# Performance work log

Hardware: AMD Instinct MI355X
Metric: run time of the kernel (lower is better)

The kernel has to match this reference:

```python
import jax, jax.numpy as jnp
import numpy as np

HIDDEN = 2048
NUM_HEADS = 16
NUM_KV_HEADS = 8
HEAD_DIM = 128
EPS = 1e-6
ROPE_THETA = 10000.0
Q_SIZE = NUM_HEADS * HEAD_DIM
KV_SIZE = NUM_KV_HEADS * HEAD_DIM


def setup_inputs() -> dict:
    key = jax.random.key(0)
    k1, k2, k3 = jax.random.split(key, 3)
    B, S = 2, 2048
    positions = jnp.broadcast_to(jnp.arange(S, dtype=jnp.int32), (B, S))
    hidden_states = jax.random.normal(k1, (B, S, HIDDEN), dtype=jnp.float32)
    w_qkv = jax.random.normal(k2, (Q_SIZE + 2 * KV_SIZE, HIDDEN), dtype=jnp.float32) * (HIDDEN ** -0.5)
    w_o = jax.random.normal(k3, (HIDDEN, Q_SIZE), dtype=jnp.float32) * (Q_SIZE ** -0.5)
    q_norm_w = jnp.ones((HEAD_DIM,), dtype=jnp.float32)
    k_norm_w = jnp.ones((HEAD_DIM,), dtype=jnp.float32)
    return {"positions": positions, "hidden_states": hidden_states,
            "w_qkv": w_qkv, "w_o": w_o, "q_norm_w": q_norm_w, "k_norm_w": k_norm_w}


def _rms_norm(x, w):
    # x: [..., HEAD_DIM]
    var = jnp.mean(x * x, axis=-1, keepdims=True)
    return x * jax.lax.rsqrt(var + EPS) * w


def _rope(x, cos, sin):
    # x: [B, S, H, D]; cos/sin: [B, S, 1, D/2] (neox style: rotate half)
    x1, x2 = jnp.split(x, 2, axis=-1)
    return jnp.concatenate([x1 * cos - x2 * sin, x2 * cos + x1 * sin], axis=-1)


def reference(positions, hidden_states, w_qkv, w_o, q_norm_w, k_norm_w):
    B, S, _ = hidden_states.shape
    qkv = jnp.einsum("bsh,oh->bso", hidden_states, w_qkv)
    q, k, v = jnp.split(qkv, [Q_SIZE, Q_SIZE + KV_SIZE], axis=-1)
    q = q.reshape(B, S, NUM_HEADS, HEAD_DIM)
    k = k.reshape(B, S, NUM_KV_HEADS, HEAD_DIM)
    v = v.reshape(B, S, NUM_KV_HEADS, HEAD_DIM)

    # per-head RMSNorm on q and k (Qwen3 qk-norm)
    q = _rms_norm(q, q_norm_w)
    k = _rms_norm(k, k_norm_w)

    # RoPE (neox style)
    inv_freq = 1.0 / (ROPE_THETA ** (jnp.arange(0, HEAD_DIM, 2, dtype=jnp.float32) / HEAD_DIM))
    angles = positions.astype(jnp.float32)[..., None] * inv_freq  # [B, S, D/2]
    cos = jnp.cos(angles)[:, :, None, :]
    sin = jnp.sin(angles)[:, :, None, :]
    q = _rope(q, cos, sin)
    k = _rope(k, cos, sin)

    # GQA: expand kv heads to match q heads
    rep = NUM_HEADS // NUM_KV_HEADS
    k = jnp.repeat(k, rep, axis=2)  # [B, S, H, D]
    v = jnp.repeat(v, rep, axis=2)

    scale = HEAD_DIM ** -0.5
    scores = jnp.einsum("bqhd,bkhd->bhqk", q, k) * scale
    causal = jnp.tril(jnp.ones((S, S), dtype=bool))
    scores = jnp.where(causal, scores, jnp.finfo(scores.dtype).min)
    probs = jax.nn.softmax(scores, axis=-1)
    attn = jnp.einsum("bhqk,bkhd->bqhd", probs, v).reshape(B, S, Q_SIZE)
    return jnp.einsum("bso,ho->bsh", attn, w_o)
```

## Files before the change

kernel.cpp:

```cpp
#include <hip/hip_runtime.h>
#include <hip/hip_bf16.h>
#include <cstdint>
#include <cstddef>

#define HIDDEN 2048
#define NHEADS 16
#define NKV    8
#define HD     128
#define QS     (NHEADS*HD)
#define KVS    (NKV*HD)
#define OC     (QS + 2*KVS)
#define BB     2
#define SS     2048
#define ROWS   (BB*SS)

typedef __bf16 bf16;
typedef __bf16 bf16x8 __attribute__((ext_vector_type(8)));
typedef __bf16 bf16x4 __attribute__((ext_vector_type(4)));
typedef float  f32x4  __attribute__((ext_vector_type(4)));
typedef float  f32x2  __attribute__((ext_vector_type(2)));
typedef int    i32x4  __attribute__((ext_vector_type(4)));

__global__ __launch_bounds__(256) void k_cvt(const float* __restrict__ src,
                                             bf16* __restrict__ dst, int n8) {
  int i = blockIdx.x * blockDim.x + threadIdx.x;
  int stride = gridDim.x * blockDim.x;
  for (; i < n8; i += stride) {
    const f32x4* s = (const f32x4*)(src + (size_t)i * 8);
    f32x4 a = s[0], b = s[1];
    bf16x8 o;
    o[0]=(bf16)a[0]; o[1]=(bf16)a[1]; o[2]=(bf16)a[2]; o[3]=(bf16)a[3];
    o[4]=(bf16)b[0]; o[5]=(bf16)b[1]; o[6]=(bf16)b[2]; o[7]=(bf16)b[3];
    *(bf16x8*)(dst + (size_t)i * 8) = o;
  }
}

__global__ __launch_bounds__(256) void k_table(float* __restrict__ tbl) {
  int t = blockIdx.x * blockDim.x + threadIdx.x;
  int pos = t >> 6, i = t & 63;
  float freq = powf(10000.0f, -(float)i / 64.0f);
  float ang = (float)pos * freq;
  float sv, cv;
  sincosf(ang, &sv, &cv);
  f32x2 v; v[0] = cv; v[1] = sv;
  ((f32x2*)tbl)[t] = v;
}

__device__ __forceinline__ void gll16(const void* g, void* l) {
  __builtin_amdgcn_global_load_lds((const __attribute__((address_space(1))) void*)g,
                                   (__attribute__((address_space(3))) void*)l, 16, 0, 0);
}

template <typename OT>
__global__ __launch_bounds__(256) void k_gemm(const bf16* __restrict__ A,
                                              const bf16* __restrict__ Bw,
                                              OT* __restrict__ C,
                                              int M, int N, int K) {
  const int tid = threadIdx.x;
  const int lane = tid & 63;
  const int w = tid >> 6;
  const int m0 = blockIdx.y * 128, n0 = blockIdx.x * 128;
  __shared__ bf16 As[128 * 64];
  __shared__ bf16 Bs[128 * 64];
  f32x4 acc[4][4] = {};
  const int wm = (w >> 1) * 64, wn = (w & 1) * 64;
  const int lr = lane & 15, lg = lane >> 4;
  const int KT = K >> 6;
  for (int kt = 0; kt < KT; ++kt) {
    __syncthreads();
    #pragma unroll
    for (int i = 0; i < 4; ++i) {
      int c = tid + i * 256;
      int row = c >> 3, kc = c & 7;
      int ch = kc ^ (row & 7);
      gll16(A + (size_t)(m0 + row) * K + kt * 64 + ch * 8, As + (size_t)(c & ~63) * 8);
      gll16(Bw + (size_t)(n0 + row) * K + kt * 64 + ch * 8, Bs + (size_t)(c & ~63) * 8);
    }
    asm volatile("s_waitcnt vmcnt(0)" ::: "memory");
    __syncthreads();
    #pragma unroll
    for (int kh = 0; kh < 2; ++kh) {
      bf16x8 af[4], bfv[4];
      #pragma unroll
      for (int i = 0; i < 4; ++i) {
        int row = wm + i * 16 + lr;
        af[i] = *(const bf16x8*)((char*)As + ((row * 128 + kh * 64 + lg * 16) ^ ((lr & 7) << 4)));
      }
      #pragma unroll
      for (int j = 0; j < 4; ++j) {
        int row = wn + j * 16 + lr;
        bfv[j] = *(const bf16x8*)((char*)Bs + ((row * 128 + kh * 64 + lg * 16) ^ ((lr & 7) << 4)));
      }
      #pragma unroll
      for (int i = 0; i < 4; ++i)
        #pragma unroll
        for (int j = 0; j < 4; ++j)
          acc[i][j] = __builtin_amdgcn_mfma_f32_16x16x32_bf16(af[i], bfv[j], acc[i][j], 0, 0, 0);
    }
  }
  for (int i = 0; i < 4; ++i)
    for (int j = 0; j < 4; ++j) {
      int col = n0 + wn + j * 16 + lr;
      for (int r = 0; r < 4; ++r) {
        int row = m0 + wm + i * 16 + lg * 4 + r;
        C[(size_t)row * N + col] = (OT)acc[i][j][r];
      }
    }
}

__global__ __launch_bounds__(256) void k_ropenorm(const bf16* __restrict__ qkv,
                                                  bf16* __restrict__ qb, bf16* __restrict__ kb,
                                                  const float* __restrict__ tbl,
                                                  const int* __restrict__ pos,
                                                  const float* __restrict__ qw,
                                                  const float* __restrict__ kw) {
  int gw = blockIdx.x * 4 + (threadIdx.x >> 6);
  int lane = threadIdx.x & 63;
  int h = gw % 24;
  int rem = gw / 24;
  int s = rem & (SS - 1);
  int b = rem >> 11;
  size_t row = (size_t)b * SS + s;
  int col0 = (h < 16) ? h * HD : QS + (h - 16) * HD;
  unsigned u = *(const unsigned*)(qkv + row * OC + col0 + lane * 2);
  float x0 = __uint_as_float((u & 0xffffu) << 16);
  float x1 = __uint_as_float(u & 0xffff0000u);
  float ssq = x0 * x0 + x1 * x1;
  for (int m = 1; m < 64; m <<= 1) ssq += __shfl_xor(ssq, m, 64);
  float r = rsqrtf(ssq * (1.0f / 128.0f) + 1e-6f);
  const float* wv = (h < 16) ? qw : kw;
  float y0 = x0 * r * wv[lane * 2], y1 = x1 * r * wv[lane * 2 + 1];
  float p0 = __shfl_xor(y0, 32, 64), p1 = __shfl_xor(y1, 32, 64);
  int p = pos[row];
  f32x4 cs = *(const f32x4*)(tbl + (size_t)p * 128 + (lane & 31) * 4);
  float o0, o1;
  if (lane < 32) { o0 = y0 * cs[0] - p0 * cs[1]; o1 = y1 * cs[2] - p1 * cs[3]; }
  else           { o0 = y0 * cs[0] + p0 * cs[1]; o1 = y1 * cs[2] + p1 * cs[3]; }
  bf16* dst; size_t drow;
  if (h < 16) { dst = qb; drow = ((size_t)b * NHEADS + h) * SS + s; }
  else        { dst = kb; drow = ((size_t)b * NKV + (h - 16)) * SS + s; }
  bf16 v0 = (bf16)o0, v1 = (bf16)o1;
  unsigned short q0, q1;
  __builtin_memcpy(&q0, &v0, 2); __builtin_memcpy(&q1, &v1, 2);
  *(unsigned*)(dst + drow * HD + lane * 2) = (unsigned)q0 | ((unsigned)q1 << 16);
}

__global__ __launch_bounds__(256) void k_vt(const bf16* __restrict__ qkv,
                                            bf16* __restrict__ vT) {
  __shared__ bf16 T[64 * 136];
  int tid = threadIdx.x;
  int st = blockIdx.x, kv = blockIdx.y, b = blockIdx.z;
  int s0 = st * 64;
  for (int i = 0; i < 4; ++i) {
    int c = tid + i * 256;
    int sl = c >> 4, dc = c & 15;
    i32x4 v = *(const i32x4*)(qkv + (size_t)(b * SS + s0 + sl) * OC + QS + KVS + kv * HD + dc * 8);
    *(i32x4*)(T + sl * 136 + dc * 8) = v;
  }
  __syncthreads();
  for (int i = 0; i < 4; ++i) {
    int c = tid + i * 256;
    int d = c >> 3, sg = c & 7;
    bf16x8 o;
    for (int j = 0; j < 8; ++j) o[j] = T[(sg * 8 + j) * 136 + d];
    *(bf16x8*)(vT + ((size_t)(b * NKV + kv) * HD + d) * SS + s0 + sg * 8) = o;
  }
}

__global__ __launch_bounds__(256) void k_attn9(const bf16* __restrict__ qb,
                                               const bf16* __restrict__ kb,
                                               const bf16* __restrict__ vT,
                                               bf16* __restrict__ out) {
  __shared__ bf16 Kl[64 * 128];
  __shared__ bf16 Vl[128 * 64];
  __shared__ bf16 Pl[4][16 * 64];
  const int tid = threadIdx.x, lane = tid & 63, w = tid >> 6;
  const int qt = gridDim.x - 1 - blockIdx.x;
  const int h = blockIdx.y, b = blockIdx.z;
  const int kvh = h >> 1;
  const int lr = lane & 15, lg = lane >> 4;
  const int qbase = qt * 64 + w * 16;
  const float NEG = -3.0e38f;
  bf16x8 qf[4];
  {
    const bf16* qrow = qb + ((size_t)(b * NHEADS + h) * SS + qbase + lr) * HD;
    #pragma unroll
    for (int ks = 0; ks < 4; ++ks) qf[ks] = *(const bf16x8*)(qrow + ks * 32 + lg * 8);
  }
  f32x4 acc[8] = {};
  float m_r = NEG, l_r = 0.0f;
  const bf16* Kg = kb + (size_t)(b * NKV + kvh) * SS * HD;
  const bf16* Vg = vT + (size_t)(b * NKV + kvh) * HD * SS;
  for (int t = 0; t <= qt; ++t) {
    const int kv0 = t * 64;
    __syncthreads();
    #pragma unroll
    for (int i = 0; i < 4; ++i) {
      int c = tid + i * 256;
      int r_ = c >> 4;
      int ch = (c & 15) ^ (r_ & 7);
      gll16(Kg + (size_t)(kv0 + r_) * HD + ch * 8, Kl + (size_t)(c & ~63) * 8);
    }
    #pragma unroll
    for (int i = 0; i < 4; ++i) {
      int c = tid + i * 256;
      int d = c >> 3;
      int ch = (c & 7) ^ (d & 7);
      gll16(Vg + (size_t)d * SS + kv0 + ch * 8, Vl + (size_t)(c & ~63) * 8);
    }
    asm volatile("s_waitcnt vmcnt(0)" ::: "memory");
    __syncthreads();
    f32x4 sf[4];
    __builtin_amdgcn_s_setprio(1);
    #pragma unroll
    for (int mt = 0; mt < 4; ++mt) {
      f32x4 a_ = {0.f, 0.f, 0.f, 0.f};
      const int rrow = mt * 16 + lr;
      #pragma unroll
      for (int ks = 0; ks < 4; ++ks) {
        bf16x8 kf = *(const bf16x8*)((char*)Kl + ((rrow * 256 + ks * 64 + lg * 16) ^ ((rrow & 7) << 4)));
        a_ = __builtin_amdgcn_mfma_f32_16x16x32_bf16(kf, qf[ks], a_, 0, 0, 0);
      }
      sf[mt] = a_;
    }
    __builtin_amdgcn_s_setprio(0);
    const float scl = 0.08838834764831845f;
    const int qg = qbase + lr;
    float pm = NEG;
    #pragma unroll
    for (int mt = 0; mt < 4; ++mt)
      #pragma unroll
      for (int r = 0; r < 4; ++r) {
        int kvg = kv0 + mt * 16 + lg * 4 + r;
        float v = sf[mt][r] * scl;
        if (kvg > qg) v = NEG;
        sf[mt][r] = v;
        pm = fmaxf(pm, v);
      }
    pm = fmaxf(pm, __shfl_xor(pm, 16, 64));
    pm = fmaxf(pm, __shfl_xor(pm, 32, 64));
    if (!__all(pm <= m_r + 8.0f)) {
      const float mn = fmaxf(m_r, pm);
      const float scale = __expf(m_r - mn);
      float sr[4];
      #pragma unroll
      for (int r = 0; r < 4; ++r) sr[r] = __shfl(scale, lg * 4 + r, 64);
      #pragma unroll
      for (int nt = 0; nt < 8; ++nt)
        #pragma unroll
        for (int r = 0; r < 4; ++r) acc[nt][r] *= sr[r];
      l_r *= scale;
      m_r = mn;
    }
    float ts = 0.f;
    #pragma unroll
    for (int mt = 0; mt < 4; ++mt)
      #pragma unroll
      for (int r = 0; r < 4; ++r) {
        float pv = __expf(sf[mt][r] - m_r);
        sf[mt][r] = pv;
        ts += pv;
      }
    ts += __shfl_xor(ts, 16, 64);
    ts += __shfl_xor(ts, 32, 64);
    l_r += ts;
    #pragma unroll
    for (int mt = 0; mt < 4; ++mt) {
      bf16x4 pk;
      #pragma unroll
      for (int r = 0; r < 4; ++r) pk[r] = (bf16)sf[mt][r];
      *(bf16x4*)((char*)&Pl[w][0] + ((lr * 128 + mt * 32 + lg * 8) ^ ((lr & 7) << 4))) = pk;
    }
    __builtin_amdgcn_s_setprio(1);
    #pragma unroll
    for (int kk = 0; kk < 2; ++kk) {
      bf16x8 pa = *(const bf16x8*)((char*)&Pl[w][0] + ((lr * 128 + kk * 64 + lg * 16) ^ ((lr & 7) << 4)));
      #pragma unroll
      for (int nt = 0; nt < 8; ++nt) {
        const int d = nt * 16 + lr;
        bf16x8 vbf = *(const bf16x8*)((char*)Vl + ((d * 128 + kk * 64 + lg * 16) ^ ((d & 7) << 4)));
        acc[nt] = __builtin_amdgcn_mfma_f32_16x16x32_bf16(pa, vbf, acc[nt], 0, 0, 0);
      }
    }
    __builtin_amdgcn_s_setprio(0);
  }
  const float inv = 1.0f / l_r;
  float ir[4];
  #pragma unroll
  for (int r = 0; r < 4; ++r) ir[r] = __shfl(inv, lg * 4 + r, 64);
  #pragma unroll
  for (int nt = 0; nt < 8; ++nt)
    #pragma unroll
    for (int r = 0; r < 4; ++r) {
      size_t row = (size_t)b * SS + qbase + lg * 4 + r;
      out[row * QS + h * HD + nt * 16 + lr] = (bf16)(acc[nt][r] * ir[r]);
    }
}

extern "C" void kernel_launch(void* const* d_in, const int* in_sizes, int n_in,
                              void* d_out, int out_size, void* d_ws, size_t ws_size,
                              hipStream_t stream) {
  const int*   pos  = (const int*)d_in[0];
  const float* hid  = (const float*)d_in[1];
  const float* wqkv = (const float*)d_in[2];
  const float* wo   = (const float*)d_in[3];
  const float* qw   = (const float*)d_in[4];
  const float* kw   = (const float*)d_in[5];
  char* ws = (char*)d_ws;
  bf16* hid_bf  = (bf16*)(ws + 0);
  bf16* attn_o  = hid_bf;
  bf16* wqkv_bf = (bf16*)(ws + 16777216);
  bf16* q_buf   = wqkv_bf;
  bf16* k_buf   = (bf16*)(ws + 33554432);
  bf16* wo_bf   = k_buf;
  bf16* qkv     = (bf16*)(ws + 41943040);
  bf16* vT      = (bf16*)(ws + 75497472);
  float* tbl    = (float*)(ws + 83886080);

  k_cvt<<<dim3(2048), dim3(256), 0, stream>>>(hid,  hid_bf,  ROWS * HIDDEN / 8);
  k_cvt<<<dim3(2048), dim3(256), 0, stream>>>(wqkv, wqkv_bf, OC * HIDDEN / 8);
  k_table<<<dim3(512), dim3(256), 0, stream>>>(tbl);
  k_gemm<bf16><<<dim3(OC / 128, ROWS / 128), dim3(256), 0, stream>>>(
      hid_bf, wqkv_bf, qkv, ROWS, OC, HIDDEN);
  k_ropenorm<<<dim3(ROWS * 24 / 4), dim3(256), 0, stream>>>(
      qkv, q_buf, k_buf, tbl, pos, qw, kw);
  k_vt<<<dim3(SS / 64, NKV, BB), dim3(256), 0, stream>>>(qkv, vT);
  k_attn9<<<dim3(SS / 64, NHEADS, BB), dim3(256), 0, stream>>>(
      q_buf, k_buf, vT, attn_o);
  k_cvt<<<dim3(2048), dim3(256), 0, stream>>>(wo, wo_bf, HIDDEN * QS / 8);
  k_gemm<float><<<dim3(HIDDEN / 128, ROWS / 128), dim3(256), 0, stream>>>(
      attn_o, wo_bf, (float*)d_out, ROWS, HIDDEN, QS);
}
```

Baseline: 302.8 us.

## Use 32x32 MFMA in GEMM, exp2 softmax, and merge conversion launches

```diff
diff --git a/kernel.cpp b/kernel.cpp
--- a/kernel.cpp
+++ b/kernel.cpp
@@ -19,6 +19,7 @@
 typedef __bf16 bf16x4 __attribute__((ext_vector_type(4)));
 typedef float  f32x4  __attribute__((ext_vector_type(4)));
 typedef float  f32x2  __attribute__((ext_vector_type(2)));
+typedef float  f32x16 __attribute__((ext_vector_type(16)));
 typedef int    i32x4  __attribute__((ext_vector_type(4)));
 
 __global__ __launch_bounds__(256) void k_cvt(const float* __restrict__ src,
@@ -35,6 +36,24 @@
   }
 }
 
+__global__ __launch_bounds__(256) void k_cvt2(const float* __restrict__ s0, bf16* __restrict__ d0, int n0,
+                                              const float* __restrict__ s1, bf16* __restrict__ d1, int n1) {
+  int i = blockIdx.x * blockDim.x + threadIdx.x;
+  int stride = gridDim.x * blockDim.x;
+  int total = n0 + n1;
+  for (; i < total; i += stride) {
+    const float* src; bf16* dst; int k;
+    if (i < n0) { src = s0; dst = d0; k = i; }
+    else        { src = s1; dst = d1; k = i - n0; }
+    const f32x4* s = (const f32x4*)(src + (size_t)k * 8);
+    f32x4 a = s[0], b = s[1];
+    bf16x8 o;
+    o[0]=(bf16)a[0]; o[1]=(bf16)a[1]; o[2]=(bf16)a[2]; o[3]=(bf16)a[3];
+    o[4]=(bf16)b[0]; o[5]=(bf16)b[1]; o[6]=(bf16)b[2]; o[7]=(bf16)b[3];
+    *(bf16x8*)(dst + (size_t)k * 8) = o;
+  }
+}
+
 __global__ __launch_bounds__(256) void k_table(float* __restrict__ tbl) {
   int t = blockIdx.x * blockDim.x + threadIdx.x;
   int pos = t >> 6, i = t & 63;
@@ -62,9 +81,9 @@
   const int m0 = blockIdx.y * 128, n0 = blockIdx.x * 128;
   __shared__ bf16 As[128 * 64];
   __shared__ bf16 Bs[128 * 64];
-  f32x4 acc[4][4] = {};
+  f32x16 acc[2][2] = {};
   const int wm = (w >> 1) * 64, wn = (w & 1) * 64;
-  const int lr = lane & 15, lg = lane >> 4;
+  const int l31 = lane & 31, hg = lane >> 5;
   const int KT = K >> 6;
   for (int kt = 0; kt < KT; ++kt) {
     __syncthreads();
@@ -78,32 +97,38 @@
     }
     asm volatile("s_waitcnt vmcnt(0)" ::: "memory");
     __syncthreads();
-    #pragma unroll
-    for (int kh = 0; kh < 2; ++kh) {
-      bf16x8 af[4], bfv[4];
-      #pragma unroll
-      for (int i = 0; i < 4; ++i) {
-        int row = wm + i * 16 + lr;
-        af[i] = *(const bf16x8*)((char*)As + ((row * 128 + kh * 64 + lg * 16) ^ ((lr & 7) << 4)));
-      }
-      #pragma unroll
-      for (int j = 0; j < 4; ++j) {
-        int row = wn + j * 16 + lr;
-        bfv[j] = *(const bf16x8*)((char*)Bs + ((row * 128 + kh * 64 + lg * 16) ^ ((lr & 7) << 4)));
-      }
-      #pragma unroll
-      for (int i = 0; i < 4; ++i)
+    bf16x8 af[2][4], bfv[2][4];
+    #pragma unroll
+    for (int i = 0; i < 2; ++i)
+      #pragma unroll
+      for (int s = 0; s < 4; ++s) {
+        int arow = wm + i * 32 + l31;
+        af[i][s] = *(const bf16x8*)((char*)As + ((arow * 128 + s * 32 + hg * 16) ^ ((arow & 7) << 4)));
+      }
+    #pragma unroll
+    for (int j = 0; j < 2; ++j)
+      #pragma unroll
+      for (int s = 0; s < 4; ++s) {
+        int brow = wn + j * 32 + l31;
+        bfv[j][s] = *(const bf16x8*)((char*)Bs + ((brow * 128 + s * 32 + hg * 16) ^ ((brow & 7) << 4)));
+      }
+    #pragma unroll
+    for (int i = 0; i < 2; ++i)
+      #pragma unroll
+      for (int j = 0; j < 2; ++j)
         #pragma unroll
-        for (int j = 0; j < 4; ++j)
-          acc[i][j] = __builtin_amdgcn_mfma_f32_16x16x32_bf16(af[i], bfv[j], acc[i][j], 0, 0, 0);
-    }
-  }
-  for (int i = 0; i < 4; ++i)
-    for (int j = 0; j < 4; ++j) {
-      int col = n0 + wn + j * 16 + lr;
-      for (int r = 0; r < 4; ++r) {
-        int row = m0 + wm + i * 16 + lg * 4 + r;
-        C[(size_t)row * N + col] = (OT)acc[i][j][r];
+        for (int s = 0; s < 4; ++s)
+          acc[i][j] = __builtin_amdgcn_mfma_f32_32x32x16_bf16(af[i][s], bfv[j][s], acc[i][j], 0, 0, 0);
+  }
+  #pragma unroll
+  for (int i = 0; i < 2; ++i)
+    #pragma unroll
+    for (int j = 0; j < 2; ++j) {
+      int col = n0 + wn + j * 32 + l31;
+      #pragma unroll
+      for (int reg = 0; reg < 16; ++reg) {
+        int row = m0 + wm + i * 32 + 4 * hg + (reg & 3) + 8 * (reg >> 2);
+        C[(size_t)row * N + col] = (OT)acc[i][j][reg];
       }
     }
 }
@@ -224,7 +249,7 @@
       sf[mt] = a_;
     }
     __builtin_amdgcn_s_setprio(0);
-    const float scl = 0.08838834764831845f;
+    const float scl2 = 0.12753102f;
     const int qg = qbase + lr;
     float pm = NEG;
     #pragma unroll
@@ -232,16 +257,16 @@
       #pragma unroll
       for (int r = 0; r < 4; ++r) {
         int kvg = kv0 + mt * 16 + lg * 4 + r;
-        float v = sf[mt][r] * scl;
+        float v = sf[mt][r] * scl2;
         if (kvg > qg) v = NEG;
         sf[mt][r] = v;
         pm = fmaxf(pm, v);
       }
     pm = fmaxf(pm, __shfl_xor(pm, 16, 64));
     pm = fmaxf(pm, __shfl_xor(pm, 32, 64));
-    if (!__all(pm <= m_r + 8.0f)) {
+    if (!__all(pm <= m_r + 11.5415603f)) {
       const float mn = fmaxf(m_r, pm);
-      const float scale = __expf(m_r - mn);
+      const float scale = exp2f(m_r - mn);
       float sr[4];
       #pragma unroll
       for (int r = 0; r < 4; ++r) sr[r] = __shfl(scale, lg * 4 + r, 64);
@@ -257,7 +282,7 @@
     for (int mt = 0; mt < 4; ++mt)
       #pragma unroll
       for (int r = 0; r < 4; ++r) {
-        float pv = __expf(sf[mt][r] - m_r);
+        float pv = exp2f(sf[mt][r] - m_r);
         sf[mt][r] = pv;
         ts += pv;
       }
@@ -317,8 +342,9 @@
   bf16* vT      = (bf16*)(ws + 75497472);
   float* tbl    = (float*)(ws + 83886080);
 
-  k_cvt<<<dim3(2048), dim3(256), 0, stream>>>(hid,  hid_bf,  ROWS * HIDDEN / 8);
-  k_cvt<<<dim3(2048), dim3(256), 0, stream>>>(wqkv, wqkv_bf, OC * HIDDEN / 8);
+  k_cvt2<<<dim3(2048), dim3(256), 0, stream>>>(
+      hid, hid_bf, ROWS * HIDDEN / 8,
+      wqkv, wqkv_bf, OC * HIDDEN / 8);
   k_table<<<dim3(512), dim3(256), 0, stream>>>(tbl);
   k_gemm<bf16><<<dim3(OC / 128, ROWS / 128), dim3(256), 0, stream>>>(
       hid_bf, wqkv_bf, qkv, ROWS, OC, HIDDEN);
```

After: 312.3 us. +3.1%, slower.
